# Kernel optimization log

Hardware: AMD Instinct MI355X
Metric: run time of the kernel (lower is better)

The kernel has to match this reference:

```python
import jax, jax.numpy as jnp
import numpy as np

N_HEADS = 16
KEY_DIM = 64
VAL_DIM = 64
HIDDEN = 1024
SCALE = 1.0 / float(KEY_DIM) ** 0.5


def setup_inputs() -> dict:
    key = jax.random.key(0)
    ks = jax.random.split(key, 16)
    B, Lq, Lk, R = 2, 2048, 2048, 2048
    inp = {
        "query": jax.random.normal(ks[0], (B, Lq, HIDDEN), jnp.float32),
        "value": jax.random.normal(ks[1], (B, Lk, HIDDEN), jnp.float32),
        "positional_embedding": jax.random.normal(ks[2], (R, HIDDEN), jnp.float32),
        "u_weight": jax.random.normal(ks[3], (N_HEADS, KEY_DIM), jnp.float32) * 0.02,
        "v_weight": jax.random.normal(ks[4], (N_HEADS, KEY_DIM), jnp.float32) * 0.02,
        "indices": jax.random.randint(ks[5], (2, Lq, Lk), 0, R, jnp.int64 if jax.config.jax_enable_x64 else jnp.int32),
        "lower": jax.random.uniform(ks[6], (Lq, Lk), jnp.float32),
    }
    s = 0.02
    inp["Wq"] = jax.random.normal(ks[7], (HIDDEN, N_HEADS * KEY_DIM), jnp.float32) * s
    inp["bq"] = jnp.zeros((N_HEADS * KEY_DIM,), jnp.float32)
    inp["Wk"] = jax.random.normal(ks[8], (HIDDEN, N_HEADS * KEY_DIM), jnp.float32) * s
    inp["bk"] = jnp.zeros((N_HEADS * KEY_DIM,), jnp.float32)
    inp["Wv"] = jax.random.normal(ks[9], (HIDDEN, N_HEADS * VAL_DIM), jnp.float32) * s
    inp["bv"] = jnp.zeros((N_HEADS * VAL_DIM,), jnp.float32)
    inp["Wr"] = jax.random.normal(ks[10], (HIDDEN, N_HEADS * KEY_DIM), jnp.float32) * s
    inp["br"] = jnp.zeros((N_HEADS * KEY_DIM,), jnp.float32)
    inp["Wo"] = jax.random.normal(ks[11], (N_HEADS * VAL_DIM, HIDDEN), jnp.float32) * s
    inp["bo"] = jnp.zeros((HIDDEN,), jnp.float32)
    return inp


def reference(query, value, positional_embedding, u_weight, v_weight, indices, lower,
              Wq, bq, Wk, bk, Wv, bv, Wr, br, Wo, bo):
    B, Lq, _ = query.shape
    Lk = value.shape[1]
    R = positional_embedding.shape[0]
    # projections (torch Linear with weights stored as [in, out])
    q = (query @ Wq + bq).reshape(B, Lq, N_HEADS, KEY_DIM)
    k = (value @ Wk + bk).reshape(B, Lk, N_HEADS, KEY_DIM)
    v = (value @ Wv + bv).reshape(B, Lk, N_HEADS, VAL_DIM)
    r = (positional_embedding @ Wr + br).reshape(R, N_HEADS, KEY_DIM)
    # content (AC) and position (BD) score terms -> [i, j, b, n]
    AC = jnp.einsum("bind,bjnd->ijbn", q + u_weight, k)
    BD = jnp.einsum("bind,jnd->ijbn", q + v_weight, r)
    # rel-shift: gather [Lq, R] -> [Lq, Lk] positions, then apply lower mask
    BD = BD[indices[0], indices[1]] * lower[:, :, None, None]
    attn = jax.nn.softmax((AC + BD) * SCALE, axis=1)  # softmax over key dim j
    out = jnp.einsum("ijbn,bjnd->bind", attn, v).reshape(B, Lq, N_HEADS * VAL_DIM)
    return out @ Wo + bo
```

## Files before the change

kernel.cpp:

```cpp
#include <hip/hip_runtime.h>
#include <stdint.h>

typedef __attribute__((ext_vector_type(8))) short short8;
typedef __attribute__((ext_vector_type(4))) float f32x4;
typedef unsigned short u16;
typedef unsigned int u32;
typedef unsigned long long u64;

#define LQ 2048
#define LK 2048
#define RDIM 2048
#define HID 1024
#define NH 16
#define DH 64
#define S2SCALE 0.1803368801111204f

__device__ __forceinline__ float bf2f(u16 u){
  union { unsigned int i; float f; } v; v.i = ((unsigned int)u) << 16; return v.f;
}
__device__ __forceinline__ u16 f2bf(float f){
  union { float f; unsigned int i; } v; v.f = f;
  unsigned int r = v.i + 0x7fffu + ((v.i >> 16) & 1u);
  return (u16)(r >> 16);
}
__device__ __forceinline__ f32x4 fzero(){ f32x4 z = {0.0f, 0.0f, 0.0f, 0.0f}; return z; }

__global__ void k_detect(const u32* __restrict__ q, const u32* __restrict__ idxw,
                         int* __restrict__ flags){
  int t = threadIdx.x;
  u32 w = q[t];
  int b = (w >> 7) & 0xFF;
  unsigned long long mb = __ballot(b >= 100 && b <= 140);
  u32 hi = idxw[2 * t + 1];
  unsigned long long mi = __ballot(hi == 0u);
  if (t == 0){
    flags[0] = (__popcll(mb) >= 48) ? 1 : 0;
    flags[1] = (__popcll(mi) == 64) ? 1 : 0;
  }
}

struct Seg { const void* src; u16* dst; int n4; };
struct SegPack { Seg s[8]; };
__global__ void k_ingestN(SegPack p, const int* __restrict__ flags){
  int f = flags[0];
  Seg sg = p.s[blockIdx.y];
  int stride = gridDim.x * blockDim.x;
  for (int i = blockIdx.x * blockDim.x + threadIdx.x; i < sg.n4; i += stride){
    if (f){
      reinterpret_cast<uint2*>(sg.dst)[i] = reinterpret_cast<const uint2*>(sg.src)[i];
    } else {
      float4 v = reinterpret_cast<const float4*>(sg.src)[i];
      union { u16 h[4]; uint2 u; } t;
      t.h[0] = f2bf(v.x); t.h[1] = f2bf(v.y); t.h[2] = f2bf(v.z); t.h[3] = f2bf(v.w);
      reinterpret_cast<uint2*>(sg.dst)[i] = t.u;
    }
  }
}

struct WPack { const void* src[5]; u16* dst[5]; };
__global__ void k_wtrans(WPack p, const int* __restrict__ flags){
  int f = flags[0];
  const void* W = p.src[blockIdx.z];
  u16* Wt = p.dst[blockIdx.z];
  __shared__ u16 t[64][65];
  int tid = threadIdx.x;
  int bx = blockIdx.x, by = blockIdx.y;
#pragma unroll
  for (int it = 0; it < 16; ++it){
    int id = it * 256 + tid;
    int r = id >> 6, c = id & 63;
    size_t so = (size_t)(by * 64 + r) * HID + bx * 64 + c;
    t[r][c] = f ? ((const u16*)W)[so] : f2bf(((const float*)W)[so]);
  }
  __syncthreads();
#pragma unroll
  for (int it = 0; it < 16; ++it){
    int id = it * 256 + tid;
    int r = id >> 6, c = id & 63;
    Wt[(size_t)(bx * 64 + r) * HID + by * 64 + c] = t[c][r];
  }
}

__global__ void k_goff(const int* __restrict__ idx, int* __restrict__ goff,
                       const int* __restrict__ flags){
  int i64f = flags[1];
  const size_t N = (size_t)LQ * LK;
  size_t stride = (size_t)gridDim.x * blockDim.x;
  for (size_t t = (size_t)blockIdx.x * blockDim.x + threadIdx.x; t < N; t += stride){
    long long a0, a1;
    if (i64f){
      const long long* ip = (const long long*)idx;
      a0 = ip[t]; a1 = ip[N + t];
    } else {
      a0 = idx[t]; a1 = idx[N + t];
    }
    goff[t] = (int)(a0 * RDIM + a1);
  }
}

__global__ void k_gemm(const u16* __restrict__ A, const u16* __restrict__ Bt,
                       const u16* __restrict__ bias,
                       const u16* __restrict__ add0, const u16* __restrict__ add1,
                       void* __restrict__ D0, u16* __restrict__ D1,
                       int headmajor, const int* __restrict__ oflags){
  __shared__ u16 As[128][72];
  __shared__ u16 Bs[128][72];
  int tid = threadIdx.x;
  int l = tid & 63, w = tid >> 6;
  int lr = l & 15, g = l >> 4;
  int wr = w >> 1, wc = w & 1;
  int outf32 = oflags ? (oflags[0] == 0) : 0;
  f32x4 acc[4][4];
#pragma unroll
  for (int a = 0; a < 4; ++a)
#pragma unroll
    for (int bq_ = 0; bq_ < 4; ++bq_) acc[a][bq_] = fzero();
  const size_t arowg = (size_t)blockIdx.x * 128;
  const size_t browg = (size_t)blockIdx.y * 128;
  for (int kt = 0; kt < HID; kt += 64){
#pragma unroll
    for (int it = 0; it < 4; ++it){
      int id = it * 256 + tid;
      int r = id >> 3, ch = id & 7;
      uint4 va = *reinterpret_cast<const uint4*>(A + (arowg + r) * HID + kt + ch * 8);
      *reinterpret_cast<uint4*>(&As[r][ch * 8]) = va;
      uint4 vb = *reinterpret_cast<const uint4*>(Bt + (browg + r) * HID + kt + ch * 8);
      *reinterpret_cast<uint4*>(&Bs[r][ch * 8]) = vb;
    }
    __syncthreads();
#pragma unroll
    for (int ks = 0; ks < 2; ++ks){
      short8 af[4], bfv[4];
#pragma unroll
      for (int mf = 0; mf < 4; ++mf)
        af[mf] = *reinterpret_cast<const short8*>(&As[wr * 64 + mf * 16 + lr][ks * 32 + 8 * g]);
#pragma unroll
      for (int nf = 0; nf < 4; ++nf)
        bfv[nf] = *reinterpret_cast<const short8*>(&Bs[wc * 64 + nf * 16 + lr][ks * 32 + 8 * g]);
#pragma unroll
      for (int mf = 0; mf < 4; ++mf)
#pragma unroll
        for (int nf = 0; nf < 4; ++nf)
          acc[mf][nf] = __builtin_amdgcn_mfma_f32_16x16x32_bf16(af[mf], bfv[nf], acc[mf][nf], 0, 0, 0);
    }
    __syncthreads();
  }
#pragma unroll
  for (int mf = 0; mf < 4; ++mf)
#pragma unroll
    for (int nf = 0; nf < 4; ++nf){
      int col = (int)browg + wc * 64 + nf * 16 + lr;
      float bcol = bf2f(bias[col]);
      float a0 = add0 ? bf2f(add0[col]) : 0.0f;
      float a1 = add1 ? bf2f(add1[col]) : 0.0f;
#pragma unroll
      for (int reg = 0; reg < 4; ++reg){
        int row = (int)arowg + wr * 64 + mf * 16 + 4 * g + reg;
        float base = acc[mf][nf][reg] + bcol;
        if (headmajor == 2){
          int b = row >> 11, i = row & 2047;
          int n32 = col >> 6, d = col & 63;
          u16* Dx = (n32 < NH) ? (u16*)D0 : D1;
          size_t dst = ((size_t)(b * NH + (n32 & (NH - 1))) * LQ + i) * DH + d;
          Dx[dst] = f2bf(base);
        } else if (headmajor == 1){
          int b = row >> 11, i = row & 2047;
          int n = col >> 6, d = col & 63;
          size_t dst = ((size_t)(b * NH + n) * LQ + i) * DH + d;
          ((u16*)D0)[dst] = f2bf(base + a0);
          if (D1) D1[dst] = f2bf(base + a1);
        } else {
          size_t dst = (size_t)row * HID + col;
          if (outf32) ((float*)D0)[dst] = base;
          else        ((u16*)D0)[dst] = f2bf(base);
        }
      }
    }
}

__global__ void k_bdfull16(const u16* __restrict__ qv, const u16* __restrict__ rr,
                           u16* __restrict__ bdf, int bnBase){
  __shared__ u16 tile[32][64][16];
  int tid = threadIdx.x;
  int l = tid & 63, w = tid >> 6;
  int lr = l & 15, g = l >> 4;
  int i0 = blockIdx.x * 32, j0 = blockIdx.y * 64;
#pragma unroll
  for (int hh = 0; hh < 4; ++hh){
    int g_ = w * 4 + hh;
    int bn = bnBase + g_;
    int b = bn >> 4, n = bn & 15;
    const u16* qb = qv + ((size_t)(b * NH + n) * LQ + i0) * DH;
    const u16* rb = rr + ((size_t)n * RDIM + j0) * DH;
    short8 af[2][2];
#pragma unroll
    for (int mf = 0; mf < 2; ++mf)
#pragma unroll
      for (int ks = 0; ks < 2; ++ks)
        af[mf][ks] = *reinterpret_cast<const short8*>(qb + (size_t)(mf * 16 + lr) * DH + ks * 32 + 8 * g);
    f32x4 acc[2][4];
#pragma unroll
    for (int mf = 0; mf < 2; ++mf)
#pragma unroll
      for (int nf = 0; nf < 4; ++nf) acc[mf][nf] = fzero();
#pragma unroll
    for (int nf = 0; nf < 4; ++nf){
#pragma unroll
      for (int ks = 0; ks < 2; ++ks){
        short8 bb = *reinterpret_cast<const short8*>(rb + (size_t)(nf * 16 + lr) * DH + ks * 32 + 8 * g);
#pragma unroll
        for (int mf = 0; mf < 2; ++mf)
          acc[mf][nf] = __builtin_amdgcn_mfma_f32_16x16x32_bf16(af[mf][ks], bb, acc[mf][nf], 0, 0, 0);
      }
    }
#pragma unroll
    for (int mf = 0; mf < 2; ++mf)
#pragma unroll
      for (int nf = 0; nf < 4; ++nf)
#pragma unroll
        for (int reg = 0; reg < 4; ++reg)
          tile[mf * 16 + 4 * g + reg][nf * 16 + lr][g_] = f2bf(acc[mf][nf][reg]);
  }
  __syncthreads();
#pragma unroll
  for (int e = 0; e < 32; ++e){
    int id = e * 256 + tid;
    int line = id >> 2, part = id & 3;
    int ii = line >> 6, jj = line & 63;
    u64 v = *reinterpret_cast<const u64*>(&tile[ii][jj][part * 4]);
    *reinterpret_cast<u64*>(
        bdf + ((size_t)(i0 + ii) * RDIM + (size_t)(j0 + jj)) * 16 + part * 4) = v;
  }
}

__global__ void k_bdfull8(const u16* __restrict__ qv, const u16* __restrict__ rr,
                          u16* __restrict__ bdf, int bnBase){
  __shared__ u16 tile[32][64][8];
  int tid = threadIdx.x;
  int l = tid & 63, w = tid >> 6;
  int lr = l & 15, g = l >> 4;
  int i0 = blockIdx.x * 32, j0 = blockIdx.y * 64;
#pragma unroll
  for (int hh = 0; hh < 2; ++hh){
    int g_ = w * 2 + hh;
    int bn = bnBase + g_;
    int b = bn >> 4, n = bn & 15;
    const u16* qb = qv + ((size_t)(b * NH + n) * LQ + i0) * DH;
    const u16* rb = rr + ((size_t)n * RDIM + j0) * DH;
    short8 af[2][2];
#pragma unroll
    for (int mf = 0; mf < 2; ++mf)
#pragma unroll
      for (int ks = 0; ks < 2; ++ks)
        af[mf][ks] = *reinterpret_cast<const short8*>(qb + (size_t)(mf * 16 + lr) * DH + ks * 32 + 8 * g);
    f32x4 acc[2][4];
#pragma unroll
    for (int mf = 0; mf < 2; ++mf)
#pragma unroll
      for (int nf = 0; nf < 4; ++nf) acc[mf][nf] = fzero();
#pragma unroll
    for (int nf = 0; nf < 4; ++nf){
#pragma unroll
      for (int ks = 0; ks < 2; ++ks){
        short8 bb = *reinterpret_cast<const short8*>(rb + (size_t)(nf * 16 + lr) * DH + ks * 32 + 8 * g);
#pragma unroll
        for (int mf = 0; mf < 2; ++mf)
          acc[mf][nf] = __builtin_amdgcn_mfma_f32_16x16x32_bf16(af[mf][ks], bb, acc[mf][nf], 0, 0, 0);
      }
    }
#pragma unroll
    for (int mf = 0; mf < 2; ++mf)
#pragma unroll
      for (int nf = 0; nf < 4; ++nf)
#pragma unroll
        for (int reg = 0; reg < 4; ++reg)
          tile[mf * 16 + 4 * g + reg][nf * 16 + lr][g_] = f2bf(acc[mf][nf][reg]);
  }
  __syncthreads();
#pragma unroll
  for (int e = 0; e < 16; ++e){
    int id = e * 256 + tid;
    int line = id >> 1, part = id & 1;
    int ii = line >> 6, jj = line & 63;
    u64 v = *reinterpret_cast<const u64*>(&tile[ii][jj][part * 4]);
    *reinterpret_cast<u64*>(
        bdf + ((size_t)(i0 + ii) * RDIM + (size_t)(j0 + jj)) * 8 + part * 4) = v;
  }
}

template<int G>
__global__ void k_bdfull(const u16* __restrict__ qv, const u16* __restrict__ rr,
                         u16* __restrict__ bdf, int bnBase){
  __shared__ u16 tile[16][32][G];
  int tid = threadIdx.x;
  int l = tid & 63, w = tid >> 6;
  int lr = l & 15, g = l >> 4;
  int i0 = blockIdx.x * 16, j0 = blockIdx.y * 32;
  if (w < G){
    int g_ = w;
    int bn = bnBase + g_;
    int b = bn >> 4, n = bn & 15;
    const u16* qb = qv + ((size_t)(b * NH + n) * LQ + i0) * DH;
    const u16* rb = rr + ((size_t)n * RDIM + j0) * DH;
    f32x4 acc2[2];
    acc2[0] = fzero(); acc2[1] = fzero();
#pragma unroll
    for (int ks = 0; ks < 2; ++ks){
      short8 a = *reinterpret_cast<const short8*>(qb + (size_t)lr * DH + ks * 32 + 8 * g);
#pragma unroll
      for (int nf = 0; nf < 2; ++nf){
        short8 bb = *reinterpret_cast<const short8*>(rb + (size_t)(lr + 16 * nf) * DH + ks * 32 + 8 * g);
        acc2[nf] = __builtin_amdgcn_mfma_f32_16x16x32_bf16(a, bb, acc2[nf], 0, 0, 0);
      }
    }
#pragma unroll
    for (int nf = 0; nf < 2; ++nf){
      int jj = lr + 16 * nf;
#pragma unroll
      for (int reg = 0; reg < 4; ++reg)
        tile[4 * g + reg][jj][g_] = f2bf(acc2[nf][reg]);
    }
  }
  __syncthreads();
  constexpr int CHUNKS = 512;
#pragma unroll
  for (int e = 0; e < (CHUNKS * G + 255) / 256 && e * 256 < CHUNKS * G; ++e){
    int id = e * 256 + tid;
    if (id >= CHUNKS * G) break;
    int line = id / G, k = id % G;
    int ii = line >> 5, jj = line & 31;
    bdf[((size_t)(i0 + ii) * RDIM + (size_t)(j0 + jj)) * G + k] = tile[ii][jj][k];
  }
}

template<int G>
__global__ void k_gather(const u16* __restrict__ bdf, const int* __restrict__ goff,
                         const u16* __restrict__ lower, u16* __restrict__ bdg){
  __shared__ u16 tile[G][16][32];
  int tid = threadIdx.x;
  int i0 = blockIdx.x * 16, j0 = blockIdx.y * 32;
#pragma unroll
  for (int it = 0; it < 2; ++it){
    int p = it * 256 + tid;
    int ii = p >> 5, jj = p & 31;
    size_t off = (size_t)(i0 + ii) * LK + (j0 + jj);
    int go = goff[off];
    float lw = bf2f(lower[off]);
    const u16* src = bdf + (size_t)go * G;
    union { uint4 q[2]; u32 w2[8]; u16 h[16]; } uv;
    if (G == 16){
      uv.q[0] = *reinterpret_cast<const uint4*>(src);
      uv.q[1] = *reinterpret_cast<const uint4*>(src + 8);
    } else if (G == 8){
      uv.q[0] = *reinterpret_cast<const uint4*>(src);
    } else if (G == 2){
      uv.w2[0] = *reinterpret_cast<const u32*>(src);
    } else {
      uv.h[0] = *src;
    }
#pragma unroll
    for (int k = 0; k < G; ++k)
      tile[k][ii][jj] = f2bf(bf2f(uv.h[k]) * lw);
  }
  __syncthreads();
  constexpr int CHUNKS = G * 128;
#pragma unroll
  for (int e = 0; e < (CHUNKS + 255) / 256; ++e){
    int id = e * 256 + tid;
    if (CHUNKS < 256 * ((CHUNKS + 255) / 256) && id >= CHUNKS) break;
    int g_ = id >> 7, rem = id & 127;
    int ii = rem >> 3, part = rem & 7;
    u64 v = *reinterpret_cast<const u64*>(&tile[g_][ii][part * 4]);
    __builtin_nontemporal_store(v, reinterpret_cast<u64*>(
        bdg + (size_t)g_ * LQ * LK + (size_t)(i0 + ii) * LK + j0 + part * 4));
  }
}

__device__ __forceinline__ void flash_compute(
    const u16 (&bd)[8][4], int lr, int g,
    const short8& aq0, const short8& aq1,
    f32x4* O, float* mrun, float* lacc,
    u16 (*klds)[72], u16 (*vtlds)[128], u16 (*pldsw)[136]){
  float sv[8][4];
#pragma unroll
  for (int nf = 0; nf < 8; ++nf){
    f32x4 z = fzero();
    short8 bk0 = *reinterpret_cast<const short8*>(&klds[lr + 16 * nf][8 * g]);
    short8 bk1 = *reinterpret_cast<const short8*>(&klds[lr + 16 * nf][32 + 8 * g]);
    z = __builtin_amdgcn_mfma_f32_16x16x32_bf16(aq0, bk0, z, 0, 0, 0);
    z = __builtin_amdgcn_mfma_f32_16x16x32_bf16(aq1, bk1, z, 0, 0, 0);
#pragma unroll
    for (int reg = 0; reg < 4; ++reg)
      sv[nf][reg] = (z[reg] + bf2f(bd[nf][reg])) * S2SCALE;
  }
  float fs[4];
#pragma unroll
  for (int reg = 0; reg < 4; ++reg){
    float mx = sv[0][reg];
#pragma unroll
    for (int nf = 1; nf < 8; ++nf) mx = fmaxf(mx, sv[nf][reg]);
#pragma unroll
    for (int d = 1; d < 16; d <<= 1) mx = fmaxf(mx, __shfl_xor(mx, d));
    float mnew = fmaxf(mrun[reg], mx);
    fs[reg] = exp2f(mrun[reg] - mnew);
    mrun[reg] = mnew;
    float sumloc = 0.0f;
#pragma unroll
    for (int nf = 0; nf < 8; ++nf){
      sv[nf][reg] = exp2f(sv[nf][reg] - mnew);
      sumloc += sv[nf][reg];
    }
    lacc[reg] = lacc[reg] * fs[reg] + sumloc;
  }
#pragma unroll
  for (int nf = 0; nf < 4; ++nf)
#pragma unroll
    for (int reg = 0; reg < 4; ++reg)
      O[nf][reg] *= fs[reg];
#pragma unroll
  for (int nf = 0; nf < 8; ++nf)
#pragma unroll
    for (int reg = 0; reg < 4; ++reg)
      pldsw[4 * g + reg][lr + 16 * nf] = f2bf(sv[nf][reg]);
  short8 pa[4];
#pragma unroll
  for (int ks = 0; ks < 4; ++ks)
    pa[ks] = *reinterpret_cast<const short8*>(&pldsw[lr][ks * 32 + 8 * g]);
#pragma unroll
  for (int nf = 0; nf < 4; ++nf){
    int d = lr + 16 * nf;
#pragma unroll
    for (int ks = 0; ks < 4; ++ks){
      int cv = ((ks * 4 + g) ^ (d >> 3)) * 8;
      short8 bv = *reinterpret_cast<const short8*>(&vtlds[d][cv]);
      O[nf] = __builtin_amdgcn_mfma_f32_16x16x32_bf16(pa[ks], bv, O[nf], 0, 0, 0);
    }
  }
}

__global__ __launch_bounds__(256) void k_flash(
    const u16* __restrict__ qu, const u16* __restrict__ kk,
    const u16* __restrict__ vv, const u16* __restrict__ bdg,
    u16* __restrict__ oo, int bnBase){
  __shared__ u16 klds[128][72];
  __shared__ u16 vtlds[64][128];
  __shared__ u16 plds[4][16][136];
  int tid = threadIdx.x;
  int l = tid & 63, w = tid >> 6;
  int lr = l & 15, g = l >> 4;
  int gi = blockIdx.x;
  int bn = bnBase + gi;
  int b = bn >> 4, n = bn & 15;
  int i0 = blockIdx.y * 64;
  const u16* qb = qu + ((size_t)bn * LQ + i0 + w * 16) * DH;
  short8 aq0 = *reinterpret_cast<const short8*>(qb + (size_t)lr * DH + 8 * g);
  short8 aq1 = *reinterpret_cast<const short8*>(qb + (size_t)lr * DH + 32 + 8 * g);
  f32x4 O[4];
#pragma unroll
  for (int nf = 0; nf < 4; ++nf) O[nf] = fzero();
  float mrun[4], lacc[4];
#pragma unroll
  for (int r = 0; r < 4; ++r){ mrun[r] = -1e30f; lacc[r] = 0.0f; }
  const u16* kbase = kk + (size_t)bn * LK * DH;
  const u16* vbase = vv + (size_t)bn * LK * DH;
  const u16* bdw = bdg + (size_t)gi * LQ * LK + (size_t)(i0 + w * 16) * LK;
  u16 (*pldsw)[136] = plds[w];

  uint4 kv[8];
  u16 bdA[8][4], bdB[8][4];

#define LOADKV(J_) do { _Pragma("unroll") for (int it_ = 0; it_ < 4; ++it_){ \
    int id_ = it_ * 256 + tid; int r_ = id_ >> 3, ch_ = id_ & 7; \
    kv[it_]     = *reinterpret_cast<const uint4*>(kbase + (size_t)((J_) + r_) * DH + ch_ * 8); \
    kv[4 + it_] = *reinterpret_cast<const uint4*>(vbase + (size_t)((J_) + r_) * DH + ch_ * 8); } } while(0)

#define WRITELDS() do { _Pragma("unroll") for (int it_ = 0; it_ < 4; ++it_){ \
    int id_ = it_ * 256 + tid; int r_ = id_ >> 3, ch_ = id_ & 7; \
    *reinterpret_cast<uint4*>(&klds[r_][ch_ * 8]) = kv[it_]; \
    u16 tmp_[8]; *reinterpret_cast<uint4*>(tmp_) = kv[4 + it_]; \
    int cb_ = r_ ^ (ch_ * 8); \
    _Pragma("unroll") for (int e_ = 0; e_ < 8; ++e_) vtlds[ch_ * 8 + e_][cb_] = tmp_[e_]; } } while(0)

#define LOADBD(B_, J_) do { _Pragma("unroll") for (int nf_ = 0; nf_ < 8; ++nf_) \
    { _Pragma("unroll") for (int rg_ = 0; rg_ < 4; ++rg_) \
      B_[nf_][rg_] = bdw[(size_t)(4 * g + rg_) * LK + (J_) + lr + 16 * nf_]; } } while(0)

  LOADKV(0); LOADBD(bdA, 0);
  WRITELDS();
  __syncthreads();

  for (int tp = 0; tp < 8; ++tp){
    int jA = tp * 256, jB = jA + 128;
    LOADKV(jB); LOADBD(bdB, jB);
    flash_compute(bdA, lr, g, aq0, aq1, O, mrun, lacc, klds, vtlds, pldsw);
    __syncthreads();
    WRITELDS();
    __syncthreads();
    if (tp < 7){ LOADKV(jA + 256); LOADBD(bdA, jA + 256); }
    flash_compute(bdB, lr, g, aq0, aq1, O, mrun, lacc, klds, vtlds, pldsw);
    if (tp < 7){
      __syncthreads();
      WRITELDS();
      __syncthreads();
    }
  }
#undef LOADKV
#undef WRITELDS
#undef LOADBD

  float lsum[4];
#pragma unroll
  for (int reg = 0; reg < 4; ++reg){
    float s = lacc[reg];
#pragma unroll
    for (int d = 1; d < 16; d <<= 1) s += __shfl_xor(s, d);
    lsum[reg] = s;
  }
#pragma unroll
  for (int nf = 0; nf < 4; ++nf)
#pragma unroll
    for (int reg = 0; reg < 4; ++reg){
      int i = i0 + w * 16 + 4 * g + reg;
      float vo = O[nf][reg] / lsum[reg];
      oo[((size_t)(b * LQ + i)) * HID + n * DH + lr + 16 * nf] = f2bf(vo);
    }
}

extern "C" void kernel_launch(void* const* d_in, const int* in_sizes, int n_in,
                              void* d_out, int out_size, void* d_ws, size_t ws_size,
                              hipStream_t stream){
  const void* query = d_in[0];
  const void* value = d_in[1];
  const void* pos   = d_in[2];
  const void* uw    = d_in[3];
  const void* vw    = d_in[4];
  const int* idx    = (const int*)d_in[5];
  const void* lower = d_in[6];
  const void* Wq = d_in[7];  const void* bq = d_in[8];
  const void* Wk = d_in[9];  const void* bk = d_in[10];
  const void* Wv = d_in[11]; const void* bv = d_in[12];
  const void* Wr = d_in[13]; const void* br = d_in[14];
  const void* Wo = d_in[15]; const void* bo = d_in[16];
  (void)in_sizes; (void)n_in; (void)out_size;

  char* ws = (char*)d_ws;
  const size_t MB = (size_t)1 << 20;
  u16* cquery = (u16*)(ws + 0 * MB);
  u16* cvalue = (u16*)(ws + 8 * MB);
  int* goff   = (int*)(ws + 0 * MB);
  u16* cpos   = (u16*)(ws + 16 * MB);
  u16* clower = (u16*)(ws + 20 * MB);
  char* sm = ws + 38 * MB;
  u16* cuw = (u16*)(sm + 0 * 4096);
  u16* cvw = (u16*)(sm + 1 * 4096);
  u16* cbq = (u16*)(sm + 2 * 4096);
  u16* cbk = (u16*)(sm + 3 * 4096);
  u16* cbv = cbk + 1024;
  u16* cbr = (u16*)(sm + 5 * 4096);
  u16* cbo = (u16*)(sm + 6 * 4096);
  int* flags = (int*)(sm + 7 * 4096);
  u16* wqt = (u16*)(ws + 39 * MB);
  u16* wkt = (u16*)(ws + 41 * MB);
  u16* wvt = (u16*)(ws + 43 * MB);
  u16* wrt = (u16*)(ws + 45 * MB);
  u16* wot = (u16*)(ws + 47 * MB);
  u16* qu  = (u16*)(ws + 49 * MB);
  u16* qv  = (u16*)(ws + 57 * MB);
  u16* kkp = (u16*)(ws + 65 * MB);
  u16* vvp = (u16*)(ws + 73 * MB);
  u16* rrp = (u16*)(ws + 81 * MB);
  u16* oo  = (u16*)(ws + 85 * MB);
  u16* bdf = (u16*)(ws + 96 * MB);

  dim3 blk(256);
  k_detect<<<1, 64, 0, stream>>>((const u32*)query, (const u32*)idx, flags);

  {
    SegPack big;
    big.s[0] = { query, cquery, 2 * LQ * HID / 4 };
    big.s[1] = { value, cvalue, 2 * LK * HID / 4 };
    big.s[2] = { pos,   cpos,   RDIM * HID / 4 };
    big.s[3] = { lower, clower, LQ * LK / 4 };
    for (int i = 4; i < 8; ++i) big.s[i] = { nullptr, nullptr, 0 };
    k_ingestN<<<dim3(512, 4), blk, 0, stream>>>(big, flags);
    SegPack sml;
    sml.s[0] = { uw, cuw, NH * DH / 4 };
    sml.s[1] = { vw, cvw, NH * DH / 4 };
    sml.s[2] = { bq, cbq, HID / 4 };
    sml.s[3] = { bk, cbk, HID / 4 };
    sml.s[4] = { bv, cbv, HID / 4 };
    sml.s[5] = { br, cbr, HID / 4 };
    sml.s[6] = { bo, cbo, HID / 4 };
    sml.s[7] = { nullptr, nullptr, 0 };
    k_ingestN<<<dim3(4, 7), blk, 0, stream>>>(sml, flags);
  }
  {
    WPack wp;
    wp.src[0] = Wq; wp.dst[0] = wqt;
    wp.src[1] = Wk; wp.dst[1] = wkt;
    wp.src[2] = Wv; wp.dst[2] = wvt;
    wp.src[3] = Wr; wp.dst[3] = wrt;
    wp.src[4] = Wo; wp.dst[4] = wot;
    k_wtrans<<<dim3(16, 16, 5), blk, 0, stream>>>(wp, flags);
  }

  k_gemm<<<dim3(32, 8), blk, 0, stream>>>(cquery, wqt, cbq, cuw, cvw, qu, qv, 1, nullptr);
  k_gemm<<<dim3(32, 16), blk, 0, stream>>>(cvalue, wkt, cbk, nullptr, nullptr, kkp, vvp, 2, nullptr);
  k_gemm<<<dim3(16, 8), blk, 0, stream>>>(cpos, wrt, cbr, nullptr, nullptr, rrp, nullptr, 1, nullptr);

  k_goff<<<dim3(1024), blk, 0, stream>>>(idx, goff, flags);

  if (ws_size >= 352 * MB){
    u16* bdg = (u16*)(ws + 224 * MB);
    for (int b0 = 0; b0 < 2 * NH; b0 += 16){
      k_bdfull16<<<dim3(64, 32), blk, 0, stream>>>(qv, rrp, bdf, b0);
      k_gather<16><<<dim3(128, 64), blk, 0, stream>>>(bdf, goff, clower, bdg);
      k_flash<<<dim3(16, 32), blk, 0, stream>>>(qu, kkp, vvp, bdg, oo, b0);
    }
  } else if (ws_size >= 224 * MB){
    u16* bdg = (u16*)(ws + 160 * MB);
    for (int b0 = 0; b0 < 2 * NH; b0 += 8){
      k_bdfull8<<<dim3(64, 32), blk, 0, stream>>>(qv, rrp, bdf, b0);
      k_gather<8><<<dim3(128, 64), blk, 0, stream>>>(bdf, goff, clower, bdg);
      k_flash<<<dim3(8, 32), blk, 0, stream>>>(qu, kkp, vvp, bdg, oo, b0);
    }
  } else if (ws_size >= 128 * MB){
    u16* bdg = (u16*)(ws + 112 * MB);
    for (int b0 = 0; b0 < 2 * NH; b0 += 2){
      k_bdfull<2><<<dim3(128, 64), blk, 0, stream>>>(qv, rrp, bdf, b0);
      k_gather<2><<<dim3(128, 64), blk, 0, stream>>>(bdf, goff, clower, bdg);
      k_flash<<<dim3(2, 32), blk, 0, stream>>>(qu, kkp, vvp, bdg, oo, b0);
    }
  } else {
    u16* bdg = (u16*)(ws + 104 * MB);
    for (int b0 = 0; b0 < 2 * NH; b0 += 1){
      k_bdfull<1><<<dim3(128, 64), blk, 0, stream>>>(qv, rrp, bdf, b0);
      k_gather<1><<<dim3(128, 64), blk, 0, stream>>>(bdf, goff, clower, bdg);
      k_flash<<<dim3(1, 32), blk, 0, stream>>>(qu, kkp, vvp, bdg, oo, b0);
    }
  }
  k_gemm<<<dim3(32, 8), blk, 0, stream>>>(oo, wot, cbo, nullptr, nullptr, d_out, nullptr, 0, flags);
}
```

Before: 958.6 us.

## Split flash attention across key dimension with separate combine kernel

The flash kernel now splits the 2048 keys into four chunks of 512 along a new grid z dimension. Each block writes unnormalized fp32 partial outputs plus its running max and sum to workspace. A new combine kernel merges the four partials with log-sum-exp rescaling and writes the bf16 output. This raises the number of blocks per flash launch so more compute units are busy when few heads are batched. The cost is extra fp32 partial traffic, one more launch per group, and the partial buffer reusing the bdf region, which is only safe because bdf is consumed before flash runs.

```diff
diff --git a/kernel.cpp b/kernel.cpp
--- a/kernel.cpp
+++ b/kernel.cpp
@@ -441,7 +441,8 @@
 __global__ __launch_bounds__(256) void k_flash(
     const u16* __restrict__ qu, const u16* __restrict__ kk,
     const u16* __restrict__ vv, const u16* __restrict__ bdg,
-    u16* __restrict__ oo, int bnBase){
+    float* __restrict__ opart, float2* __restrict__ mlpart,
+    int GH, int bnBase){
   __shared__ u16 klds[128][72];
   __shared__ u16 vtlds[64][128];
   __shared__ u16 plds[4][16][136];
@@ -450,8 +451,9 @@
   int lr = l & 15, g = l >> 4;
   int gi = blockIdx.x;
   int bn = bnBase + gi;
-  int b = bn >> 4, n = bn & 15;
   int i0 = blockIdx.y * 64;
+  int z = blockIdx.z;
+  int zbase = z * 512;
   const u16* qb = qu + ((size_t)bn * LQ + i0 + w * 16) * DH;
   short8 aq0 = *reinterpret_cast<const short8*>(qb + (size_t)lr * DH + 8 * g);
   short8 aq1 = *reinterpret_cast<const short8*>(qb + (size_t)lr * DH + 32 + 8 * g);
@@ -485,20 +487,20 @@
     { _Pragma("unroll") for (int rg_ = 0; rg_ < 4; ++rg_) \
       B_[nf_][rg_] = bdw[(size_t)(4 * g + rg_) * LK + (J_) + lr + 16 * nf_]; } } while(0)
 
-  LOADKV(0); LOADBD(bdA, 0);
+  LOADKV(zbase); LOADBD(bdA, zbase);
   WRITELDS();
   __syncthreads();
 
-  for (int tp = 0; tp < 8; ++tp){
-    int jA = tp * 256, jB = jA + 128;
+  for (int tp = 0; tp < 2; ++tp){
+    int jA = zbase + tp * 256, jB = jA + 128;
     LOADKV(jB); LOADBD(bdB, jB);
     flash_compute(bdA, lr, g, aq0, aq1, O, mrun, lacc, klds, vtlds, pldsw);
     __syncthreads();
     WRITELDS();
     __syncthreads();
-    if (tp < 7){ LOADKV(jA + 256); LOADBD(bdA, jA + 256); }
+    if (tp < 1){ LOADKV(jA + 256); LOADBD(bdA, jA + 256); }
     flash_compute(bdB, lr, g, aq0, aq1, O, mrun, lacc, klds, vtlds, pldsw);
-    if (tp < 7){
+    if (tp < 1){
       __syncthreads();
       WRITELDS();
       __syncthreads();
@@ -516,14 +518,47 @@
     for (int d = 1; d < 16; d <<= 1) s += __shfl_xor(s, d);
     lsum[reg] = s;
   }
-#pragma unroll
-  for (int nf = 0; nf < 4; ++nf)
+  size_t obase = ((size_t)z * GH + gi) * LQ;
+  if (lr == 0){
 #pragma unroll
     for (int reg = 0; reg < 4; ++reg){
       int i = i0 + w * 16 + 4 * g + reg;
-      float vo = O[nf][reg] / lsum[reg];
-      oo[((size_t)(b * LQ + i)) * HID + n * DH + lr + 16 * nf] = f2bf(vo);
-    }
+      float2 ml; ml.x = mrun[reg]; ml.y = lsum[reg];
+      mlpart[obase + i] = ml;
+    }
+  }
+#pragma unroll
+  for (int nf = 0; nf < 4; ++nf)
+#pragma unroll
+    for (int reg = 0; reg < 4; ++reg){
+      int i = i0 + w * 16 + 4 * g + reg;
+      opart[(obase + i) * DH + lr + 16 * nf] = O[nf][reg];
+    }
+}
+
+__global__ void k_combine(const float* __restrict__ opart, const float2* __restrict__ mlpart,
+                          u16* __restrict__ oo, int GH, int bnBase){
+  int gi = blockIdx.x;
+  int tid = threadIdx.x;
+  int i = blockIdx.y * 4 + (tid >> 6);
+  int d = tid & 63;
+  int bn = bnBase + gi;
+  int b = bn >> 4, n = bn & 15;
+  float2 ml[4];
+  float m = -1e30f;
+#pragma unroll
+  for (int s = 0; s < 4; ++s){
+    ml[s] = mlpart[((size_t)s * GH + gi) * LQ + i];
+    m = fmaxf(m, ml[s].x);
+  }
+  float acc = 0.0f, lt = 0.0f;
+#pragma unroll
+  for (int s = 0; s < 4; ++s){
+    float sc = exp2f(ml[s].x - m);
+    lt += sc * ml[s].y;
+    acc += sc * opart[(((size_t)s * GH + gi) * LQ + i) * DH + d];
+  }
+  oo[((size_t)(b * LQ + i)) * HID + n * DH + d] = f2bf(acc / lt);
 }
 
 extern "C" void kernel_launch(void* const* d_in, const int* in_sizes, int n_in,
@@ -571,6 +606,7 @@
   u16* rrp = (u16*)(ws + 81 * MB);
   u16* oo  = (u16*)(ws + 85 * MB);
   u16* bdf = (u16*)(ws + 96 * MB);
+  float*  opart  = (float*)(ws + 96 * MB);
 
   dim3 blk(256);
   k_detect<<<1, 64, 0, stream>>>((const u32*)query, (const u32*)idx, flags);
@@ -611,32 +647,44 @@
   k_goff<<<dim3(1024), blk, 0, stream>>>(idx, goff, flags);
 
   if (ws_size >= 352 * MB){
+    int GH = 16;
     u16* bdg = (u16*)(ws + 224 * MB);
-    for (int b0 = 0; b0 < 2 * NH; b0 += 16){
+    float2* mlpart = (float2*)(ws + 96 * MB + (size_t)4 * GH * LQ * DH * 4);
+    for (int b0 = 0; b0 < 2 * NH; b0 += GH){
       k_bdfull16<<<dim3(64, 32), blk, 0, stream>>>(qv, rrp, bdf, b0);
       k_gather<16><<<dim3(128, 64), blk, 0, stream>>>(bdf, goff, clower, bdg);
-      k_flash<<<dim3(16, 32), blk, 0, stream>>>(qu, kkp, vvp, bdg, oo, b0);
+      k_flash<<<dim3(GH, 32, 4), blk, 0, stream>>>(qu, kkp, vvp, bdg, opart, mlpart, GH, b0);
+      k_combine<<<dim3(GH, 512), blk, 0, stream>>>(opart, mlpart, oo, GH, b0);
     }
   } else if (ws_size >= 224 * MB){
+    int GH = 8;
     u16* bdg = (u16*)(ws + 160 * MB);
-    for (int b0 = 0; b0 < 2 * NH; b0 += 8){
+    float2* mlpart = (float2*)(ws + 96 * MB + (size_t)4 * GH * LQ * DH * 4);
+    for (int b0 = 0; b0 < 2 * NH; b0 += GH){
       k_bdfull8<<<dim3(64, 32), blk, 0, stream>>>(qv, rrp, bdf, b0);
       k_gather<8><<<dim3(128, 64), blk, 0, stream>>>(bdf, goff, clower, bdg);
-      k_flash<<<dim3(8, 32), blk, 0, stream>>>(qu, kkp, vvp, bdg, oo, b0);
+      k_flash<<<dim3(GH, 32, 4), blk, 0, stream>>>(qu, kkp, vvp, bdg, opart, mlpart, GH, b0);
+      k_combine<<<dim3(GH, 512), blk, 0, stream>>>(opart, mlpart, oo, GH, b0);
     }
   } else if (ws_size >= 128 * MB){
+    int GH = 2;
     u16* bdg = (u16*)(ws + 112 * MB);
-    for (int b0 = 0; b0 < 2 * NH; b0 += 2){
+    float2* mlpart = (float2*)(ws + 96 * MB + (size_t)4 * GH * LQ * DH * 4);
+    for (int b0 = 0; b0 < 2 * NH; b0 += GH){
       k_bdfull<2><<<dim3(128, 64), blk, 0, stream>>>(qv, rrp, bdf, b0);
       k_gather<2><<<dim3(128, 64), blk, 0, stream>>>(bdf, goff, clower, bdg);
-      k_flash<<<dim3(2, 32), blk, 0, stream>>>(qu, kkp, vvp, bdg, oo, b0);
+      k_flash<<<dim3(GH, 32, 4), blk, 0, stream>>>(qu, kkp, vvp, bdg, opart, mlpart, GH, b0);
+      k_combine<<<dim3(GH, 512), blk, 0, stream>>>(opart, mlpart, oo, GH, b0);
     }
   } else {
+    int GH = 1;
     u16* bdg = (u16*)(ws + 104 * MB);
-    for (int b0 = 0; b0 < 2 * NH; b0 += 1){
+    float2* mlpart = (float2*)(ws + 96 * MB + (size_t)4 * GH * LQ * DH * 4);
+    for (int b0 = 0; b0 < 2 * NH; b0 += GH){
       k_bdfull<1><<<dim3(128, 64), blk, 0, stream>>>(qv, rrp, bdf, b0);
       k_gather<1><<<dim3(128, 64), blk, 0, stream>>>(bdf, goff, clower, bdg);
-      k_flash<<<dim3(1, 32), blk, 0, stream>>>(qu, kkp, vvp, bdg, oo, b0);
+      k_flash<<<dim3(GH, 32, 4), blk, 0, stream>>>(qu, kkp, vvp, bdg, opart, mlpart, GH, b0);
+      k_combine<<<dim3(GH, 512), blk, 0, stream>>>(opart, mlpart, oo, GH, b0);
     }
   }
   k_gemm<<<dim3(32, 8), blk, 0, stream>>>(oo, wot, cbo, nullptr, nullptr, d_out, nullptr, 0, flags);
```

Measured after the change: 995.1 us. +3.8%, slower.
